# Optimization experiments

Measured on AMD Instinct MI355X. Metric: run time of the kernel, lower is better.

Reference implementation:

```python
import jax, jax.numpy as jnp
import numpy as np

EPS = 1e-6

def setup_inputs() -> dict:
    key = jax.random.key(0)
    ks = jax.random.split(key, 6)
    N, E, Din, H, D = 50000, 800000, 256, 4, 32
    x = jax.random.normal(ks[0], (N, Din), dtype=jnp.float32)
    adj_indices = jax.random.randint(ks[1], (E, 2), 0, N, dtype=jnp.int32)
    adj_weights = jax.random.uniform(ks[2], (E,), dtype=jnp.float32)
    W = jax.random.normal(ks[3], (Din, H * D), dtype=jnp.float32) * (1.0 / np.sqrt(Din))
    a_src = jax.random.normal(ks[4], (H, D), dtype=jnp.float32)
    a_dst = jax.random.normal(ks[5], (H, D), dtype=jnp.float32)
    return {"x": x, "adj_indices": adj_indices, "adj_weights": adj_weights,
            "W": W, "a_src": a_src, "a_dst": a_dst}

def reference(x, adj_indices, adj_weights, W, a_src, a_dst):
    N = x.shape[0]
    H, D = a_src.shape
    h = (x @ W).reshape(N, H, D)                       # [N,H,D]
    src = adj_indices[:, 0]
    dst = adj_indices[:, 1]
    hs = h[src]                                        # [E,H,D]
    hd = h[dst]                                        # [E,H,D]
    raw = jnp.einsum('ehd,hd->eh', hs, a_src) + jnp.einsum('ehd,hd->eh', hd, a_dst)
    gate = jnp.clip(adj_weights, EPS, None)[:, None]   # [E,1]
    scores = jnp.tanh(raw) + jnp.log(gate)             # [E,H]
    # per-destination segment softmax (numerically stable)
    seg_max = jax.ops.segment_max(scores, dst, num_segments=N)   # [N,H]
    ex = jnp.exp(scores - seg_max[dst])
    denom = jax.ops.segment_sum(ex, dst, num_segments=N)         # [N,H]
    alpha = ex / denom[dst]                            # softmax over edges per dst
    alpha = alpha * gate
    messages = alpha[:, :, None] * hs                  # [E,H,D]
    out = jax.ops.segment_sum(messages, dst, num_segments=N)     # [N,H,D]
    out = out.reshape(N, H * D)
    return jax.nn.gelu(out, approximate=False)
```

## Files before the change

### kernel.cpp

```cpp
#include <hip/hip_runtime.h>
#include <hip/hip_bf16.h>

#define N_NODES 50000
#define N_EDGES 800000
#define DIN 256
#define HD 128
#define NH 4
#define CAP 64
#define CSTR 16

#define GROWS 64
#define LDKH 136

#define GEMM_BLOCKS ((N_NODES + GROWS - 1) / GROWS)
#define SCAT_BLOCKS ((N_EDGES + 255) / 256)

typedef __bf16 bf16x8 __attribute__((ext_vector_type(8)));
typedef float  f32x4  __attribute__((ext_vector_type(4)));

static __device__ __forceinline__ unsigned short f2bu(float v) {
  union { __hip_bfloat16 b; unsigned short u; } c;
  c.b = __float2bfloat16(v);
  return c.u;
}

static __device__ __forceinline__ unsigned short f2hu(float v) {
  union { _Float16 h; unsigned short u; } c;
  c.h = (_Float16)v;
  return c.u;
}

static __device__ __forceinline__ float hu2f(unsigned short u) {
  union { _Float16 h; unsigned short u; } c;
  c.u = u;
  return (float)c.h;
}

__global__ void init_kernel(const float* __restrict__ W,
                            unsigned short* __restrict__ WtF,
                            int* __restrict__ cursor) {
  int i = blockIdx.x * 256 + threadIdx.x;
  if (i < HD * DIN) {
    int j    = i & 7;
    int lane = (i >> 3) & 63;
    int t    = (i >> 9) & 7;
    int s    = (i >> 12) & 3;
    int ks   = (i >> 14) & 1;
    int m = lane & 15, q = lane >> 4;
    int k = ks * 128 + 32 * s + 8 * q + j;
    int c = 16 * t + m;
    WtF[i] = f2bu(W[k * HD + c]);
  }
  if (i < N_NODES * CSTR) cursor[i] = 0;
}

__global__ void fused_gemm_scatter(
    const float* __restrict__ x,
    const unsigned short* __restrict__ WtF,
    const float* __restrict__ a_src,
    const float* __restrict__ a_dst,
    unsigned short* __restrict__ hbf,
    float* __restrict__ ssrc,
    float* __restrict__ sdst,
    const int2* __restrict__ adj,
    const float* __restrict__ wts,
    int* __restrict__ cursor,
    unsigned int* __restrict__ slots) {
  __shared__ unsigned short xs[GROWS * LDKH];
  const int tid = threadIdx.x;

  if (blockIdx.x >= GEMM_BLOCKS) {
    int e = (blockIdx.x - GEMM_BLOCKS) * 256 + tid;
    if (e >= N_EDGES) return;
    int2 sd = adj[e];
    if ((unsigned)sd.x >= (unsigned)N_NODES || (unsigned)sd.y >= (unsigned)N_NODES) return;
    float g = fmaxf(wts[e], 1e-6f);
    int pos = atomicAdd(&cursor[sd.y * CSTR], 1);
    if (pos >= CAP) pos = CAP - 1;
    unsigned packed = ((unsigned)f2hu(g) << 16) | (unsigned)(sd.x & 0xffff);
    __builtin_nontemporal_store(packed, &slots[((size_t)sd.y << 6) + pos]);
    return;
  }

  const int row0 = blockIdx.x * GROWS;
  const int wid  = tid >> 6;
  const int lane = tid & 63;
  const int m    = lane & 15;
  const int q    = lane >> 4;

  float4 v0[8];
#pragma unroll
  for (int it = 0; it < 8; it++) {
    int i = it * 256 + tid, r = i >> 5, kq = i & 31;
    int row = row0 + r;
    v0[it] = (row < N_NODES) ? *(const float4*)(x + (size_t)row * DIN + 4 * kq)
                             : make_float4(0.f, 0.f, 0.f, 0.f);
  }
#pragma unroll
  for (int it = 0; it < 8; it++) {
    int i = it * 256 + tid, r = i >> 5, kq = i & 31;
    ushort4 b;
    b.x = f2bu(v0[it].x); b.y = f2bu(v0[it].y); b.z = f2bu(v0[it].z); b.w = f2bu(v0[it].w);
    *(ushort4*)&xs[r * LDKH + 4 * kq] = b;
  }
  __syncthreads();

  f32x4 acc[8];
#pragma unroll
  for (int t = 0; t < 8; t++) acc[t] = (f32x4){0.f, 0.f, 0.f, 0.f};

  const unsigned short* xbase = &xs[(wid * 16 + m) * LDKH];

  bf16x8 a0[4];
#pragma unroll
  for (int s = 0; s < 4; s++) a0[s] = *(const bf16x8*)(xbase + 32 * s + 8 * q);

  float4 v1[8];
#pragma unroll
  for (int it = 0; it < 8; it++) {
    int i = it * 256 + tid, r = i >> 5, kq = i & 31;
    int row = row0 + r;
    v1[it] = (row < N_NODES) ? *(const float4*)(x + (size_t)row * DIN + 128 + 4 * kq)
                             : make_float4(0.f, 0.f, 0.f, 0.f);
  }

#pragma unroll
  for (int s = 0; s < 4; s++) {
    bf16x8 bfr[8];
#pragma unroll
    for (int t = 0; t < 8; t++)
      bfr[t] = *(const bf16x8*)(WtF + (size_t)((0 * 4 + s) * 8 + t) * 512 + lane * 8);
#pragma unroll
    for (int t = 0; t < 8; t++)
      acc[t] = __builtin_amdgcn_mfma_f32_16x16x32_bf16(a0[s], bfr[t], acc[t], 0, 0, 0);
  }
  __syncthreads();

#pragma unroll
  for (int it = 0; it < 8; it++) {
    int i = it * 256 + tid, r = i >> 5, kq = i & 31;
    ushort4 b;
    b.x = f2bu(v1[it].x); b.y = f2bu(v1[it].y); b.z = f2bu(v1[it].z); b.w = f2bu(v1[it].w);
    *(ushort4*)&xs[r * LDKH + 4 * kq] = b;
  }
  __syncthreads();

  bf16x8 a1[4];
#pragma unroll
  for (int s = 0; s < 4; s++) a1[s] = *(const bf16x8*)(xbase + 32 * s + 8 * q);

#pragma unroll
  for (int s = 0; s < 4; s++) {
    bf16x8 bfr[8];
#pragma unroll
    for (int t = 0; t < 8; t++)
      bfr[t] = *(const bf16x8*)(WtF + (size_t)((1 * 4 + s) * 8 + t) * 512 + lane * 8);
#pragma unroll
    for (int t = 0; t < 8; t++)
      acc[t] = __builtin_amdgcn_mfma_f32_16x16x32_bf16(a1[s], bfr[t], acc[t], 0, 0, 0);
  }

#pragma unroll
  for (int t = 0; t < 8; t++) {
#pragma unroll
    for (int r = 0; r < 4; r++) {
      int row = row0 + wid * 16 + q * 4 + r;
      if (row < N_NODES) hbf[(size_t)row * HD + 16 * t + m] = f2bu(acc[t][r]);
    }
  }

  float as[8], ad[8];
#pragma unroll
  for (int t = 0; t < 8; t++) {
    as[t] = a_src[16 * t + m];
    ad[t] = a_dst[16 * t + m];
  }
#pragma unroll
  for (int r = 0; r < 4; r++) {
    float ps[NH] = {0.f, 0.f, 0.f, 0.f};
    float pd[NH] = {0.f, 0.f, 0.f, 0.f};
#pragma unroll
    for (int t = 0; t < 8; t++) {
      ps[t >> 1] = fmaf(acc[t][r], as[t], ps[t >> 1]);
      pd[t >> 1] = fmaf(acc[t][r], ad[t], pd[t >> 1]);
    }
#pragma unroll
    for (int mm = 8; mm >= 1; mm >>= 1) {
#pragma unroll
      for (int hh = 0; hh < NH; hh++) {
        ps[hh] += __shfl_xor(ps[hh], mm, 64);
        pd[hh] += __shfl_xor(pd[hh], mm, 64);
      }
    }
    int row = row0 + wid * 16 + q * 4 + r;
    if (m == 0 && row < N_NODES) {
#pragma unroll
      for (int hh = 0; hh < NH; hh++) {
        ssrc[row * NH + hh] = ps[hh];
        sdst[row * NH + hh] = pd[hh];
      }
    }
  }
}

__global__ __launch_bounds__(128, 4) void node_kernel(
    const int* __restrict__ cursor,
    const unsigned int* __restrict__ slots,
    const float4* __restrict__ ssrc4,
    const float4* __restrict__ sdst4,
    const unsigned int* __restrict__ hbf32,
    float* __restrict__ out) {
  const int tid  = threadIdx.x;
  const int wid  = tid >> 6;
  const int lane = tid & 63;
  const int n    = blockIdx.x * 2 + wid;
  const int hh   = lane >> 4;

  int deg = cursor[n * CSTR];
  if (deg > CAP) deg = CAP;

  __shared__ int    sidx[2][CAP];
  __shared__ float4 swv[2][CAP];

  float4 ex = make_float4(0.f, 0.f, 0.f, 0.f);
  if (lane < deg) {
    unsigned sl = slots[((size_t)n << 6) + lane];
    int s = (int)(sl & 0xffffu);
    float g = hu2f((unsigned short)(sl >> 16));
    float4 ss = ssrc4[s];
    float4 sd = sdst4[n];
    ex.x = g * expf(tanhf(ss.x + sd.x));
    ex.y = g * expf(tanhf(ss.y + sd.y));
    ex.z = g * expf(tanhf(ss.z + sd.z));
    ex.w = g * expf(tanhf(ss.w + sd.w));
    sidx[wid][lane] = s;
    swv[wid][lane] = make_float4(ex.x * g, ex.y * g, ex.z * g, ex.w * g);
  }

  float4 tot = ex;
#pragma unroll
  for (int mm = 32; mm >= 1; mm >>= 1) {
    tot.x += __shfl_xor(tot.x, mm, 64);
    tot.y += __shfl_xor(tot.y, mm, 64);
    tot.z += __shfl_xor(tot.z, mm, 64);
    tot.w += __shfl_xor(tot.w, mm, 64);
  }
  float dn  = (hh == 0) ? tot.x : (hh == 1) ? tot.y : (hh == 2) ? tot.z : tot.w;
  float inv = (dn > 0.f) ? 1.f / dn : 0.f;
  __syncthreads();

  float acc0 = 0.f, acc1 = 0.f;
  int j = 0;
  for (; j + 8 <= deg; j += 8) {
    int s0 = sidx[wid][j + 0], s1 = sidx[wid][j + 1];
    int s2 = sidx[wid][j + 2], s3 = sidx[wid][j + 3];
    int s4 = sidx[wid][j + 4], s5 = sidx[wid][j + 5];
    int s6 = sidx[wid][j + 6], s7 = sidx[wid][j + 7];
    unsigned u0 = hbf32[(size_t)s0 * (HD / 2) + lane];
    unsigned u1 = hbf32[(size_t)s1 * (HD / 2) + lane];
    unsigned u2 = hbf32[(size_t)s2 * (HD / 2) + lane];
    unsigned u3 = hbf32[(size_t)s3 * (HD / 2) + lane];
    unsigned u4 = hbf32[(size_t)s4 * (HD / 2) + lane];
    unsigned u5 = hbf32[(size_t)s5 * (HD / 2) + lane];
    unsigned u6 = hbf32[(size_t)s6 * (HD / 2) + lane];
    unsigned u7 = hbf32[(size_t)s7 * (HD / 2) + lane];
    float w0 = ((const float*)&swv[wid][j + 0])[hh];
    float w1 = ((const float*)&swv[wid][j + 1])[hh];
    float w2 = ((const float*)&swv[wid][j + 2])[hh];
    float w3 = ((const float*)&swv[wid][j + 3])[hh];
    float w4 = ((const float*)&swv[wid][j + 4])[hh];
    float w5 = ((const float*)&swv[wid][j + 5])[hh];
    float w6 = ((const float*)&swv[wid][j + 6])[hh];
    float w7 = ((const float*)&swv[wid][j + 7])[hh];
    acc0 = fmaf(w0, __uint_as_float(u0 << 16), acc0);
    acc1 = fmaf(w0, __uint_as_float(u0 & 0xffff0000u), acc1);
    acc0 = fmaf(w1, __uint_as_float(u1 << 16), acc0);
    acc1 = fmaf(w1, __uint_as_float(u1 & 0xffff0000u), acc1);
    acc0 = fmaf(w2, __uint_as_float(u2 << 16), acc0);
    acc1 = fmaf(w2, __uint_as_float(u2 & 0xffff0000u), acc1);
    acc0 = fmaf(w3, __uint_as_float(u3 << 16), acc0);
    acc1 = fmaf(w3, __uint_as_float(u3 & 0xffff0000u), acc1);
    acc0 = fmaf(w4, __uint_as_float(u4 << 16), acc0);
    acc1 = fmaf(w4, __uint_as_float(u4 & 0xffff0000u), acc1);
    acc0 = fmaf(w5, __uint_as_float(u5 << 16), acc0);
    acc1 = fmaf(w5, __uint_as_float(u5 & 0xffff0000u), acc1);
    acc0 = fmaf(w6, __uint_as_float(u6 << 16), acc0);
    acc1 = fmaf(w6, __uint_as_float(u6 & 0xffff0000u), acc1);
    acc0 = fmaf(w7, __uint_as_float(u7 << 16), acc0);
    acc1 = fmaf(w7, __uint_as_float(u7 & 0xffff0000u), acc1);
  }
  for (; j < deg; j++) {
    int s0 = sidx[wid][j];
    unsigned u0 = hbf32[(size_t)s0 * (HD / 2) + lane];
    float w0 = ((const float*)&swv[wid][j])[hh];
    acc0 = fmaf(w0, __uint_as_float(u0 << 16), acc0);
    acc1 = fmaf(w0, __uint_as_float(u0 & 0xffff0000u), acc1);
  }
  acc0 *= inv;
  acc1 *= inv;

  float2 gl;
  gl.x = 0.5f * acc0 * (1.f + erff(acc0 * 0.70710678118654752f));
  gl.y = 0.5f * acc1 * (1.f + erff(acc1 * 0.70710678118654752f));
  *(float2*)&out[(size_t)n * HD + 2 * lane] = gl;
}

extern "C" void kernel_launch(void* const* d_in, const int* in_sizes, int n_in,
                              void* d_out, int out_size, void* d_ws, size_t ws_size,
                              hipStream_t stream) {
  const float* x     = (const float*)d_in[0];
  const int2*  adj   = (const int2*)d_in[1];
  const float* wts   = (const float*)d_in[2];
  const float* W     = (const float*)d_in[3];
  const float* a_src = (const float*)d_in[4];
  const float* a_dst = (const float*)d_in[5];
  float* out = (float*)d_out;

  char* p = (char*)d_ws;
  auto carve = [&](size_t bytes) {
    char* q = p;
    p += (bytes + 255) & ~(size_t)255;
    return (void*)q;
  };
  unsigned short* hbf = (unsigned short*)carve((size_t)N_NODES * HD * sizeof(unsigned short));
  unsigned short* WtF = (unsigned short*)carve((size_t)HD * DIN * sizeof(unsigned short));
  float* ssrc   = (float*)carve((size_t)N_NODES * NH * sizeof(float));
  float* sdst   = (float*)carve((size_t)N_NODES * NH * sizeof(float));
  unsigned int* slots = (unsigned int*)carve((size_t)N_NODES * CAP * sizeof(unsigned int));
  int*   cursor = (int*)carve((size_t)N_NODES * CSTR * sizeof(int));

  init_kernel<<<(N_NODES * CSTR + 255) / 256, 256, 0, stream>>>(W, WtF, cursor);
  fused_gemm_scatter<<<GEMM_BLOCKS + SCAT_BLOCKS, 256, 0, stream>>>(
      x, WtF, a_src, a_dst, hbf, ssrc, sdst, adj, wts, cursor, slots);
  node_kernel<<<N_NODES / 2, 128, 0, stream>>>(cursor, slots, (const float4*)ssrc,
                                               (const float4*)sdst,
                                               (const unsigned int*)hbf, out);
}
```

Measured before the change: 192.3 us.

## Merge three kernels into one persistent kernel with grid barriers

Replaces the init, GEMM+scatter and per-node aggregation kernels with a single persistent kernel of 1024 blocks that loops over tasks and separates phases with software grid-wide barriers built on atomics. It also uses 4 nodes per 256-thread block in the aggregation phase and drops the nontemporal store for slots. The aim is to remove kernel launch gaps and tail effects between stages. In exchange it adds a memset, spin-wait barriers that depend on all 1024 blocks being co-resident, and lower occupancy in the gather phase than the many small blocks used before.

```diff
diff --git a/kernel.cpp b/kernel.cpp
--- a/kernel.cpp
+++ b/kernel.cpp
@@ -12,8 +12,12 @@
 #define GROWS 64
 #define LDKH 136
 
-#define GEMM_BLOCKS ((N_NODES + GROWS - 1) / GROWS)
-#define SCAT_BLOCKS ((N_EDGES + 255) / 256)
+#define GEMM_TASKS ((N_NODES + GROWS - 1) / GROWS)
+#define SCAT_TASKS (N_EDGES / 256)
+#define P1_TASKS   (GEMM_TASKS + SCAT_TASKS)
+#define NODE_TASKS (N_NODES / 4)
+
+#define NB 1024
 
 typedef __bf16 bf16x8 __attribute__((ext_vector_type(8)));
 typedef float  f32x4  __attribute__((ext_vector_type(4)));
@@ -36,273 +40,287 @@
   return (float)c.h;
 }
 
-__global__ void init_kernel(const float* __restrict__ W,
-                            unsigned short* __restrict__ WtF,
-                            int* __restrict__ cursor) {
-  int i = blockIdx.x * 256 + threadIdx.x;
-  if (i < HD * DIN) {
-    int j    = i & 7;
-    int lane = (i >> 3) & 63;
-    int t    = (i >> 9) & 7;
-    int s    = (i >> 12) & 3;
-    int ks   = (i >> 14) & 1;
-    int m = lane & 15, q = lane >> 4;
-    int k = ks * 128 + 32 * s + 8 * q + j;
-    int c = 16 * t + m;
-    WtF[i] = f2bu(W[k * HD + c]);
+static __device__ __forceinline__ void grid_barrier(unsigned int* bar, unsigned nb) {
+  __syncthreads();
+  if (threadIdx.x == 0) {
+    __threadfence();
+    unsigned arrived =
+        __hip_atomic_fetch_add(bar, 1u, __ATOMIC_ACQ_REL, __HIP_MEMORY_SCOPE_AGENT) + 1u;
+    if (arrived < nb) {
+      while (__hip_atomic_load(bar, __ATOMIC_ACQUIRE, __HIP_MEMORY_SCOPE_AGENT) < nb)
+        __builtin_amdgcn_s_sleep(2);
+    }
+    __threadfence();
   }
-  if (i < N_NODES * CSTR) cursor[i] = 0;
-}
-
-__global__ void fused_gemm_scatter(
+  __syncthreads();
+}
+
+__global__ __launch_bounds__(256, 4) void mega_kernel(
     const float* __restrict__ x,
-    const unsigned short* __restrict__ WtF,
+    const float* __restrict__ W,
     const float* __restrict__ a_src,
     const float* __restrict__ a_dst,
+    const int2* __restrict__ adj,
+    const float* __restrict__ wts,
+    unsigned short* __restrict__ WtF,
     unsigned short* __restrict__ hbf,
     float* __restrict__ ssrc,
     float* __restrict__ sdst,
-    const int2* __restrict__ adj,
-    const float* __restrict__ wts,
     int* __restrict__ cursor,
-    unsigned int* __restrict__ slots) {
-  __shared__ unsigned short xs[GROWS * LDKH];
+    unsigned int* __restrict__ slots,
+    unsigned int* __restrict__ bar,
+    float* __restrict__ out) {
+  __shared__ __align__(16) char shraw[GROWS * LDKH * 2];
   const int tid = threadIdx.x;
-
-  if (blockIdx.x >= GEMM_BLOCKS) {
-    int e = (blockIdx.x - GEMM_BLOCKS) * 256 + tid;
-    if (e >= N_EDGES) return;
-    int2 sd = adj[e];
-    if ((unsigned)sd.x >= (unsigned)N_NODES || (unsigned)sd.y >= (unsigned)N_NODES) return;
-    float g = fmaxf(wts[e], 1e-6f);
-    int pos = atomicAdd(&cursor[sd.y * CSTR], 1);
-    if (pos >= CAP) pos = CAP - 1;
-    unsigned packed = ((unsigned)f2hu(g) << 16) | (unsigned)(sd.x & 0xffff);
-    __builtin_nontemporal_store(packed, &slots[((size_t)sd.y << 6) + pos]);
-    return;
-  }
-
-  const int row0 = blockIdx.x * GROWS;
+  const int bid = blockIdx.x;
+  const unsigned nb = gridDim.x;
+
   const int wid  = tid >> 6;
   const int lane = tid & 63;
   const int m    = lane & 15;
   const int q    = lane >> 4;
 
-  float4 v0[8];
-#pragma unroll
-  for (int it = 0; it < 8; it++) {
-    int i = it * 256 + tid, r = i >> 5, kq = i & 31;
-    int row = row0 + r;
-    v0[it] = (row < N_NODES) ? *(const float4*)(x + (size_t)row * DIN + 4 * kq)
-                             : make_float4(0.f, 0.f, 0.f, 0.f);
+  for (int i = bid * 256 + tid; i < N_NODES * CSTR; i += nb * 256) cursor[i] = 0;
+  for (int i = bid * 256 + tid; i < HD * DIN; i += nb * 256) {
+    int j  = i & 7;
+    int ln = (i >> 3) & 63;
+    int t  = (i >> 9) & 7;
+    int s  = (i >> 12) & 3;
+    int ks = (i >> 14) & 1;
+    int mm = ln & 15, qq = ln >> 4;
+    WtF[i] = f2bu(W[(ks * 128 + 32 * s + 8 * qq + j) * HD + 16 * t + mm]);
   }
-#pragma unroll
-  for (int it = 0; it < 8; it++) {
-    int i = it * 256 + tid, r = i >> 5, kq = i & 31;
-    ushort4 b;
-    b.x = f2bu(v0[it].x); b.y = f2bu(v0[it].y); b.z = f2bu(v0[it].z); b.w = f2bu(v0[it].w);
-    *(ushort4*)&xs[r * LDKH + 4 * kq] = b;
+  grid_barrier(&bar[0], nb);
+
+  unsigned short* xs = (unsigned short*)shraw;
+  for (int task = bid; task < P1_TASKS; task += nb) {
+    if (task >= GEMM_TASKS) {
+      int e = (task - GEMM_TASKS) * 256 + tid;
+      int2 sd = adj[e];
+      if ((unsigned)sd.x < (unsigned)N_NODES && (unsigned)sd.y < (unsigned)N_NODES) {
+        float g = fmaxf(wts[e], 1e-6f);
+        int pos = atomicAdd(&cursor[sd.y * CSTR], 1);
+        if (pos >= CAP) pos = CAP - 1;
+        unsigned packed = ((unsigned)f2hu(g) << 16) | (unsigned)(sd.x & 0xffff);
+        slots[((size_t)sd.y << 6) + pos] = packed;
+      }
+    } else {
+      const int row0 = task * GROWS;
+
+      float4 v0[8];
+#pragma unroll
+      for (int it = 0; it < 8; it++) {
+        int i = it * 256 + tid, r = i >> 5, kq = i & 31;
+        int row = row0 + r;
+        v0[it] = (row < N_NODES) ? *(const float4*)(x + (size_t)row * DIN + 4 * kq)
+                                 : make_float4(0.f, 0.f, 0.f, 0.f);
+      }
+      __syncthreads();
+#pragma unroll
+      for (int it = 0; it < 8; it++) {
+        int i = it * 256 + tid, r = i >> 5, kq = i & 31;
+        ushort4 b;
+        b.x = f2bu(v0[it].x); b.y = f2bu(v0[it].y); b.z = f2bu(v0[it].z); b.w = f2bu(v0[it].w);
+        *(ushort4*)&xs[r * LDKH + 4 * kq] = b;
+      }
+      __syncthreads();
+
+      f32x4 acc[8];
+#pragma unroll
+      for (int t = 0; t < 8; t++) acc[t] = (f32x4){0.f, 0.f, 0.f, 0.f};
+
+      const unsigned short* xbase = &xs[(wid * 16 + m) * LDKH];
+
+      bf16x8 a0[4];
+#pragma unroll
+      for (int s = 0; s < 4; s++) a0[s] = *(const bf16x8*)(xbase + 32 * s + 8 * q);
+
+      float4 v1[8];
+#pragma unroll
+      for (int it = 0; it < 8; it++) {
+        int i = it * 256 + tid, r = i >> 5, kq = i & 31;
+        int row = row0 + r;
+        v1[it] = (row < N_NODES) ? *(const float4*)(x + (size_t)row * DIN + 128 + 4 * kq)
+                                 : make_float4(0.f, 0.f, 0.f, 0.f);
+      }
+
+#pragma unroll
+      for (int s = 0; s < 4; s++) {
+        bf16x8 bfr[8];
+#pragma unroll
+        for (int t = 0; t < 8; t++)
+          bfr[t] = *(const bf16x8*)(WtF + (size_t)((0 * 4 + s) * 8 + t) * 512 + lane * 8);
+#pragma unroll
+        for (int t = 0; t < 8; t++)
+          acc[t] = __builtin_amdgcn_mfma_f32_16x16x32_bf16(a0[s], bfr[t], acc[t], 0, 0, 0);
+      }
+      __syncthreads();
+
+#pragma unroll
+      for (int it = 0; it < 8; it++) {
+        int i = it * 256 + tid, r = i >> 5, kq = i & 31;
+        ushort4 b;
+        b.x = f2bu(v1[it].x); b.y = f2bu(v1[it].y); b.z = f2bu(v1[it].z); b.w = f2bu(v1[it].w);
+        *(ushort4*)&xs[r * LDKH + 4 * kq] = b;
+      }
+      __syncthreads();
+
+      bf16x8 a1[4];
+#pragma unroll
+      for (int s = 0; s < 4; s++) a1[s] = *(const bf16x8*)(xbase + 32 * s + 8 * q);
+
+#pragma unroll
+      for (int s = 0; s < 4; s++) {
+        bf16x8 bfr[8];
+#pragma unroll
+        for (int t = 0; t < 8; t++)
+          bfr[t] = *(const bf16x8*)(WtF + (size_t)((1 * 4 + s) * 8 + t) * 512 + lane * 8);
+#pragma unroll
+        for (int t = 0; t < 8; t++)
+          acc[t] = __builtin_amdgcn_mfma_f32_16x16x32_bf16(a1[s], bfr[t], acc[t], 0, 0, 0);
+      }
+
+#pragma unroll
+      for (int t = 0; t < 8; t++) {
+#pragma unroll
+        for (int r = 0; r < 4; r++) {
+          int row = row0 + wid * 16 + q * 4 + r;
+          if (row < N_NODES) hbf[(size_t)row * HD + 16 * t + m] = f2bu(acc[t][r]);
+        }
+      }
+
+      float as[8], ad[8];
+#pragma unroll
+      for (int t = 0; t < 8; t++) {
+        as[t] = a_src[16 * t + m];
+        ad[t] = a_dst[16 * t + m];
+      }
+#pragma unroll
+      for (int r = 0; r < 4; r++) {
+        float ps[NH] = {0.f, 0.f, 0.f, 0.f};
+        float pd[NH] = {0.f, 0.f, 0.f, 0.f};
+#pragma unroll
+        for (int t = 0; t < 8; t++) {
+          ps[t >> 1] = fmaf(acc[t][r], as[t], ps[t >> 1]);
+          pd[t >> 1] = fmaf(acc[t][r], ad[t], pd[t >> 1]);
+        }
+#pragma unroll
+        for (int mmk = 8; mmk >= 1; mmk >>= 1) {
+#pragma unroll
+          for (int hh = 0; hh < NH; hh++) {
+            ps[hh] += __shfl_xor(ps[hh], mmk, 64);
+            pd[hh] += __shfl_xor(pd[hh], mmk, 64);
+          }
+        }
+        int row = row0 + wid * 16 + q * 4 + r;
+        if (m == 0 && row < N_NODES) {
+#pragma unroll
+          for (int hh = 0; hh < NH; hh++) {
+            ssrc[row * NH + hh] = ps[hh];
+            sdst[row * NH + hh] = pd[hh];
+          }
+        }
+      }
+    }
   }
-  __syncthreads();
-
-  f32x4 acc[8];
-#pragma unroll
-  for (int t = 0; t < 8; t++) acc[t] = (f32x4){0.f, 0.f, 0.f, 0.f};
-
-  const unsigned short* xbase = &xs[(wid * 16 + m) * LDKH];
-
-  bf16x8 a0[4];
-#pragma unroll
-  for (int s = 0; s < 4; s++) a0[s] = *(const bf16x8*)(xbase + 32 * s + 8 * q);
-
-  float4 v1[8];
-#pragma unroll
-  for (int it = 0; it < 8; it++) {
-    int i = it * 256 + tid, r = i >> 5, kq = i & 31;
-    int row = row0 + r;
-    v1[it] = (row < N_NODES) ? *(const float4*)(x + (size_t)row * DIN + 128 + 4 * kq)
-                             : make_float4(0.f, 0.f, 0.f, 0.f);
+  grid_barrier(&bar[1], nb);
+
+  int*    sidx = (int*)shraw;
+  float4* swv  = (float4*)(shraw + 4 * CAP * 4);
+  const float4* ssrc4 = (const float4*)ssrc;
+  const float4* sdst4 = (const float4*)sdst;
+  const unsigned int* hbf32 = (const unsigned int*)hbf;
+  const int hh = lane >> 4;
+
+  for (int task = bid; task < NODE_TASKS; task += nb) {
+    const int n = task * 4 + wid;
+
+    int deg = cursor[n * CSTR];
+    if (deg > CAP) deg = CAP;
+
+    __syncthreads();
+
+    float4 ex = make_float4(0.f, 0.f, 0.f, 0.f);
+    if (lane < deg) {
+      unsigned sl = slots[((size_t)n << 6) + lane];
+      int s = (int)(sl & 0xffffu);
+      float g = hu2f((unsigned short)(sl >> 16));
+      float4 ss = ssrc4[s];
+      float4 sd = sdst4[n];
+      ex.x = g * expf(tanhf(ss.x + sd.x));
+      ex.y = g * expf(tanhf(ss.y + sd.y));
+      ex.z = g * expf(tanhf(ss.z + sd.z));
+      ex.w = g * expf(tanhf(ss.w + sd.w));
+      sidx[wid * CAP + lane] = s;
+      swv[wid * CAP + lane] = make_float4(ex.x * g, ex.y * g, ex.z * g, ex.w * g);
+    }
+
+    float4 tot = ex;
+#pragma unroll
+    for (int mmk = 32; mmk >= 1; mmk >>= 1) {
+      tot.x += __shfl_xor(tot.x, mmk, 64);
+      tot.y += __shfl_xor(tot.y, mmk, 64);
+      tot.z += __shfl_xor(tot.z, mmk, 64);
+      tot.w += __shfl_xor(tot.w, mmk, 64);
+    }
+    float dn  = (hh == 0) ? tot.x : (hh == 1) ? tot.y : (hh == 2) ? tot.z : tot.w;
+    float inv = (dn > 0.f) ? 1.f / dn : 0.f;
+
+    float acc0 = 0.f, acc1 = 0.f;
+    int j = 0;
+    for (; j + 8 <= deg; j += 8) {
+      int s0 = sidx[wid * CAP + j + 0], s1 = sidx[wid * CAP + j + 1];
+      int s2 = sidx[wid * CAP + j + 2], s3 = sidx[wid * CAP + j + 3];
+      int s4 = sidx[wid * CAP + j + 4], s5 = sidx[wid * CAP + j + 5];
+      int s6 = sidx[wid * CAP + j + 6], s7 = sidx[wid * CAP + j + 7];
+      unsigned u0 = hbf32[(size_t)s0 * (HD / 2) + lane];
+      unsigned u1 = hbf32[(size_t)s1 * (HD / 2) + lane];
+      unsigned u2 = hbf32[(size_t)s2 * (HD / 2) + lane];
+      unsigned u3 = hbf32[(size_t)s3 * (HD / 2) + lane];
+      unsigned u4 = hbf32[(size_t)s4 * (HD / 2) + lane];
+      unsigned u5 = hbf32[(size_t)s5 * (HD / 2) + lane];
+      unsigned u6 = hbf32[(size_t)s6 * (HD / 2) + lane];
+      unsigned u7 = hbf32[(size_t)s7 * (HD / 2) + lane];
+      float w0 = ((const float*)&swv[wid * CAP + j + 0])[hh];
+      float w1 = ((const float*)&swv[wid * CAP + j + 1])[hh];
+      float w2 = ((const float*)&swv[wid * CAP + j + 2])[hh];
+      float w3 = ((const float*)&swv[wid * CAP + j + 3])[hh];
+      float w4 = ((const float*)&swv[wid * CAP + j + 4])[hh];
+      float w5 = ((const float*)&swv[wid * CAP + j + 5])[hh];
+      float w6 = ((const float*)&swv[wid * CAP + j + 6])[hh];
+      float w7 = ((const float*)&swv[wid * CAP + j + 7])[hh];
+      acc0 = fmaf(w0, __uint_as_float(u0 << 16), acc0);
+      acc1 = fmaf(w0, __uint_as_float(u0 & 0xffff0000u), acc1);
+      acc0 = fmaf(w1, __uint_as_float(u1 << 16), acc0);
+      acc1 = fmaf(w1, __uint_as_float(u1 & 0xffff0000u), acc1);
+      acc0 = fmaf(w2, __uint_as_float(u2 << 16), acc0);
+      acc1 = fmaf(w2, __uint_as_float(u2 & 0xffff0000u), acc1);
+      acc0 = fmaf(w3, __uint_as_float(u3 << 16), acc0);
+      acc1 = fmaf(w3, __uint_as_float(u3 & 0xffff0000u), acc1);
+      acc0 = fmaf(w4, __uint_as_float(u4 << 16), acc0);
+      acc1 = fmaf(w4, __uint_as_float(u4 & 0xffff0000u), acc1);
+      acc0 = fmaf(w5, __uint_as_float(u5 << 16), acc0);
+      acc1 = fmaf(w5, __uint_as_float(u5 & 0xffff0000u), acc1);
+      acc0 = fmaf(w6, __uint_as_float(u6 << 16), acc0);
+      acc1 = fmaf(w6, __uint_as_float(u6 & 0xffff0000u), acc1);
+      acc0 = fmaf(w7, __uint_as_float(u7 << 16), acc0);
+      acc1 = fmaf(w7, __uint_as_float(u7 & 0xffff0000u), acc1);
+    }
+    for (; j < deg; j++) {
+      int s0 = sidx[wid * CAP + j];
+      unsigned u0 = hbf32[(size_t)s0 * (HD / 2) + lane];
+      float w0 = ((const float*)&swv[wid * CAP + j])[hh];
+      acc0 = fmaf(w0, __uint_as_float(u0 << 16), acc0);
+      acc1 = fmaf(w0, __uint_as_float(u0 & 0xffff0000u), acc1);
+    }
+    acc0 *= inv;
+    acc1 *= inv;
+
+    float2 gl;
+    gl.x = 0.5f * acc0 * (1.f + erff(acc0 * 0.70710678118654752f));
+    gl.y = 0.5f * acc1 * (1.f + erff(acc1 * 0.70710678118654752f));
+    *(float2*)&out[(size_t)n * HD + 2 * lane] = gl;
   }
-
-#pragma unroll
-  for (int s = 0; s < 4; s++) {
-    bf16x8 bfr[8];
-#pragma unroll
-    for (int t = 0; t < 8; t++)
-      bfr[t] = *(const bf16x8*)(WtF + (size_t)((0 * 4 + s) * 8 + t) * 512 + lane * 8);
-#pragma unroll
-    for (int t = 0; t < 8; t++)
-      acc[t] = __builtin_amdgcn_mfma_f32_16x16x32_bf16(a0[s], bfr[t], acc[t], 0, 0, 0);
-  }
-  __syncthreads();
-
-#pragma unroll
-  for (int it = 0; it < 8; it++) {
-    int i = it * 256 + tid, r = i >> 5, kq = i & 31;
-    ushort4 b;
-    b.x = f2bu(v1[it].x); b.y = f2bu(v1[it].y); b.z = f2bu(v1[it].z); b.w = f2bu(v1[it].w);
-    *(ushort4*)&xs[r * LDKH + 4 * kq] = b;
-  }
-  __syncthreads();
-
-  bf16x8 a1[4];
-#pragma unroll
-  for (int s = 0; s < 4; s++) a1[s] = *(const bf16x8*)(xbase + 32 * s + 8 * q);
-
-#pragma unroll
-  for (int s = 0; s < 4; s++) {
-    bf16x8 bfr[8];
-#pragma unroll
-    for (int t = 0; t < 8; t++)
-      bfr[t] = *(const bf16x8*)(WtF + (size_t)((1 * 4 + s) * 8 + t) * 512 + lane * 8);
-#pragma unroll
-    for (int t = 0; t < 8; t++)
-      acc[t] = __builtin_amdgcn_mfma_f32_16x16x32_bf16(a1[s], bfr[t], acc[t], 0, 0, 0);
-  }
-
-#pragma unroll
-  for (int t = 0; t < 8; t++) {
-#pragma unroll
-    for (int r = 0; r < 4; r++) {
-      int row = row0 + wid * 16 + q * 4 + r;
-      if (row < N_NODES) hbf[(size_t)row * HD + 16 * t + m] = f2bu(acc[t][r]);
-    }
-  }
-
-  float as[8], ad[8];
-#pragma unroll
-  for (int t = 0; t < 8; t++) {
-    as[t] = a_src[16 * t + m];
-    ad[t] = a_dst[16 * t + m];
-  }
-#pragma unroll
-  for (int r = 0; r < 4; r++) {
-    float ps[NH] = {0.f, 0.f, 0.f, 0.f};
-    float pd[NH] = {0.f, 0.f, 0.f, 0.f};
-#pragma unroll
-    for (int t = 0; t < 8; t++) {
-      ps[t >> 1] = fmaf(acc[t][r], as[t], ps[t >> 1]);
-      pd[t >> 1] = fmaf(acc[t][r], ad[t], pd[t >> 1]);
-    }
-#pragma unroll
-    for (int mm = 8; mm >= 1; mm >>= 1) {
-#pragma unroll
-      for (int hh = 0; hh < NH; hh++) {
-        ps[hh] += __shfl_xor(ps[hh], mm, 64);
-        pd[hh] += __shfl_xor(pd[hh], mm, 64);
-      }
-    }
-    int row = row0 + wid * 16 + q * 4 + r;
-    if (m == 0 && row < N_NODES) {
-#pragma unroll
-      for (int hh = 0; hh < NH; hh++) {
-        ssrc[row * NH + hh] = ps[hh];
-        sdst[row * NH + hh] = pd[hh];
-      }
-    }
-  }
-}
-
-__global__ __launch_bounds__(128, 4) void node_kernel(
-    const int* __restrict__ cursor,
-    const unsigned int* __restrict__ slots,
-    const float4* __restrict__ ssrc4,
-    const float4* __restrict__ sdst4,
-    const unsigned int* __restrict__ hbf32,
-    float* __restrict__ out) {
-  const int tid  = threadIdx.x;
-  const int wid  = tid >> 6;
-  const int lane = tid & 63;
-  const int n    = blockIdx.x * 2 + wid;
-  const int hh   = lane >> 4;
-
-  int deg = cursor[n * CSTR];
-  if (deg > CAP) deg = CAP;
-
-  __shared__ int    sidx[2][CAP];
-  __shared__ float4 swv[2][CAP];
-
-  float4 ex = make_float4(0.f, 0.f, 0.f, 0.f);
-  if (lane < deg) {
-    unsigned sl = slots[((size_t)n << 6) + lane];
-    int s = (int)(sl & 0xffffu);
-    float g = hu2f((unsigned short)(sl >> 16));
-    float4 ss = ssrc4[s];
-    float4 sd = sdst4[n];
-    ex.x = g * expf(tanhf(ss.x + sd.x));
-    ex.y = g * expf(tanhf(ss.y + sd.y));
-    ex.z = g * expf(tanhf(ss.z + sd.z));
-    ex.w = g * expf(tanhf(ss.w + sd.w));
-    sidx[wid][lane] = s;
-    swv[wid][lane] = make_float4(ex.x * g, ex.y * g, ex.z * g, ex.w * g);
-  }
-
-  float4 tot = ex;
-#pragma unroll
-  for (int mm = 32; mm >= 1; mm >>= 1) {
-    tot.x += __shfl_xor(tot.x, mm, 64);
-    tot.y += __shfl_xor(tot.y, mm, 64);
-    tot.z += __shfl_xor(tot.z, mm, 64);
-    tot.w += __shfl_xor(tot.w, mm, 64);
-  }
-  float dn  = (hh == 0) ? tot.x : (hh == 1) ? tot.y : (hh == 2) ? tot.z : tot.w;
-  float inv = (dn > 0.f) ? 1.f / dn : 0.f;
-  __syncthreads();
-
-  float acc0 = 0.f, acc1 = 0.f;
-  int j = 0;
-  for (; j + 8 <= deg; j += 8) {
-    int s0 = sidx[wid][j + 0], s1 = sidx[wid][j + 1];
-    int s2 = sidx[wid][j + 2], s3 = sidx[wid][j + 3];
-    int s4 = sidx[wid][j + 4], s5 = sidx[wid][j + 5];
-    int s6 = sidx[wid][j + 6], s7 = sidx[wid][j + 7];
-    unsigned u0 = hbf32[(size_t)s0 * (HD / 2) + lane];
-    unsigned u1 = hbf32[(size_t)s1 * (HD / 2) + lane];
-    unsigned u2 = hbf32[(size_t)s2 * (HD / 2) + lane];
-    unsigned u3 = hbf32[(size_t)s3 * (HD / 2) + lane];
-    unsigned u4 = hbf32[(size_t)s4 * (HD / 2) + lane];
-    unsigned u5 = hbf32[(size_t)s5 * (HD / 2) + lane];
-    unsigned u6 = hbf32[(size_t)s6 * (HD / 2) + lane];
-    unsigned u7 = hbf32[(size_t)s7 * (HD / 2) + lane];
-    float w0 = ((const float*)&swv[wid][j + 0])[hh];
-    float w1 = ((const float*)&swv[wid][j + 1])[hh];
-    float w2 = ((const float*)&swv[wid][j + 2])[hh];
-    float w3 = ((const float*)&swv[wid][j + 3])[hh];
-    float w4 = ((const float*)&swv[wid][j + 4])[hh];
-    float w5 = ((const float*)&swv[wid][j + 5])[hh];
-    float w6 = ((const float*)&swv[wid][j + 6])[hh];
-    float w7 = ((const float*)&swv[wid][j + 7])[hh];
-    acc0 = fmaf(w0, __uint_as_float(u0 << 16), acc0);
-    acc1 = fmaf(w0, __uint_as_float(u0 & 0xffff0000u), acc1);
-    acc0 = fmaf(w1, __uint_as_float(u1 << 16), acc0);
-    acc1 = fmaf(w1, __uint_as_float(u1 & 0xffff0000u), acc1);
-    acc0 = fmaf(w2, __uint_as_float(u2 << 16), acc0);
-    acc1 = fmaf(w2, __uint_as_float(u2 & 0xffff0000u), acc1);
-    acc0 = fmaf(w3, __uint_as_float(u3 << 16), acc0);
-    acc1 = fmaf(w3, __uint_as_float(u3 & 0xffff0000u), acc1);
-    acc0 = fmaf(w4, __uint_as_float(u4 << 16), acc0);
-    acc1 = fmaf(w4, __uint_as_float(u4 & 0xffff0000u), acc1);
-    acc0 = fmaf(w5, __uint_as_float(u5 << 16), acc0);
-    acc1 = fmaf(w5, __uint_as_float(u5 & 0xffff0000u), acc1);
-    acc0 = fmaf(w6, __uint_as_float(u6 << 16), acc0);
-    acc1 = fmaf(w6, __uint_as_float(u6 & 0xffff0000u), acc1);
-    acc0 = fmaf(w7, __uint_as_float(u7 << 16), acc0);
-    acc1 = fmaf(w7, __uint_as_float(u7 & 0xffff0000u), acc1);
-  }
-  for (; j < deg; j++) {
-    int s0 = sidx[wid][j];
-    unsigned u0 = hbf32[(size_t)s0 * (HD / 2) + lane];
-    float w0 = ((const float*)&swv[wid][j])[hh];
-    acc0 = fmaf(w0, __uint_as_float(u0 << 16), acc0);
-    acc1 = fmaf(w0, __uint_as_float(u0 & 0xffff0000u), acc1);
-  }
-  acc0 *= inv;
-  acc1 *= inv;
-
-  float2 gl;
-  gl.x = 0.5f * acc0 * (1.f + erff(acc0 * 0.70710678118654752f));
-  gl.y = 0.5f * acc1 * (1.f + erff(acc1 * 0.70710678118654752f));
-  *(float2*)&out[(size_t)n * HD + 2 * lane] = gl;
 }
 
 extern "C" void kernel_launch(void* const* d_in, const int* in_sizes, int n_in,
@@ -328,11 +346,9 @@
   float* sdst   = (float*)carve((size_t)N_NODES * NH * sizeof(float));
   unsigned int* slots = (unsigned int*)carve((size_t)N_NODES * CAP * sizeof(unsigned int));
   int*   cursor = (int*)carve((size_t)N_NODES * CSTR * sizeof(int));
-
-  init_kernel<<<(N_NODES * CSTR + 255) / 256, 256, 0, stream>>>(W, WtF, cursor);
-  fused_gemm_scatter<<<GEMM_BLOCKS + SCAT_BLOCKS, 256, 0, stream>>>(
-      x, WtF, a_src, a_dst, hbf, ssrc, sdst, adj, wts, cursor, slots);
-  node_kernel<<<N_NODES / 2, 128, 0, stream>>>(cursor, slots, (const float4*)ssrc,
-                                               (const float4*)sdst,
-                                               (const unsigned int*)hbf, out);
-}
+  unsigned int* bar = (unsigned int*)carve(2 * sizeof(unsigned int));
+
+  hipMemsetAsync(bar, 0, 2 * sizeof(unsigned int), stream);
+  mega_kernel<<<NB, 256, 0, stream>>>(x, W, a_src, a_dst, adj, wts, WtF, hbf,
+                                      ssrc, sdst, cursor, slots, bar, out);
+}
```

Result: slower. 653.3 us (+239.7%).
